# Kernel tuning notes

Measured on AMD Instinct MI355X. Metric: run time of the kernel, lower is better.

## Reference

```python
import jax, jax.numpy as jnp
import numpy as np

N_HEAD = 8
PREFIX_LEN = 77  # hardcoded text prefix length in the 'prefix' model_type branch
MASKED_BIAS = -10000.0


def setup_inputs() -> dict:
    key = jax.random.key(0)
    k1, k2, k3 = jax.random.split(key, 3)
    B, S, D = 8, 1024, 1024
    x = jax.random.normal(k1, (B, S, D), dtype=jnp.float32)
    attention_mask = jnp.zeros((B, 1, 1, S), dtype=jnp.float32)
    W_attn = jax.random.normal(k2, (D, 3 * D), dtype=jnp.float32) * 0.02
    b_attn = jnp.zeros((3 * D,), dtype=jnp.float32)
    W_proj = jax.random.normal(k3, (D, D), dtype=jnp.float32) * 0.02
    b_proj = jnp.zeros((D,), dtype=jnp.float32)
    return {"x": x, "attention_mask": attention_mask, "W_attn": W_attn,
            "b_attn": b_attn, "W_proj": W_proj, "b_proj": b_proj}


def _prefix_mask(S):
    # Rows < 77: attend only to cols < 77 (bidirectional prefix).
    # Rows >= 77: standard causal (cols <= row).
    row = jnp.arange(S)[:, None]
    col = jnp.arange(S)[None, :]
    return jnp.where(row < PREFIX_LEN, col < PREFIX_LEN, col <= row)  # [S, S] bool


def reference(x, attention_mask, W_attn, b_attn, W_proj, b_proj):
    B, S, D = x.shape
    H = N_HEAD
    hd = D // H
    qkv = x @ W_attn + b_attn                         # [B, S, 3D]
    q, k, v = jnp.split(qkv, 3, axis=-1)
    q = q.reshape(B, S, H, hd).transpose(0, 2, 1, 3)  # [B, H, S, hd]
    k = k.reshape(B, S, H, hd).transpose(0, 2, 1, 3)
    v = v.reshape(B, S, H, hd).transpose(0, 2, 1, 3)
    w = jnp.einsum('bhqd,bhkd->bhqk', q, k) / jnp.sqrt(jnp.float32(hd))
    mask = _prefix_mask(S)[None, None]                # [1, 1, S, S]
    w = jnp.where(mask, w, jnp.float32(MASKED_BIAS))
    w = w + attention_mask                            # additive mask [B,1,1,S]
    w = jax.nn.softmax(w, axis=-1)
    # dropout omitted (eval-mode reference)
    a = jnp.einsum('bhqk,bhkd->bhqd', w, v)           # [B, H, S, hd]
    a = a.transpose(0, 2, 1, 3).reshape(B, S, D)      # merge heads
    return a @ W_proj + b_proj
```

## Files before the change

kernel.cpp:

```cpp
#include <hip/hip_runtime.h>
#include <cstdint>
#include <cstddef>

#define B_  8
#define S_  1024
#define D_  1024
#define H_  8
#define HD_ 128
#define N3_ 3072
#define PREFIX 77
#define MASKED_BIAS -10000.0f

typedef __bf16 bf16x8 __attribute__((ext_vector_type(8)));
typedef float  f32x4  __attribute__((ext_vector_type(4)));

__device__ __forceinline__ unsigned short f2bf_rne(float f) {
    unsigned int u = __float_as_uint(f);
    u += 0x7FFFu + ((u >> 16) & 1u);
    return (unsigned short)(u >> 16);
}
__device__ __forceinline__ float bf2f(unsigned short h) {
    return __uint_as_float(((unsigned int)h) << 16);
}

__device__ __forceinline__ void load_lds16(const unsigned short* g, unsigned short* l) {
    __builtin_amdgcn_global_load_lds(
        (const __attribute__((address_space(1))) unsigned int*)g,
        (__attribute__((address_space(3))) unsigned int*)l,
        16, 0, 0);
}

__global__ void prep(const float* __restrict__ x, unsigned short* __restrict__ xb,
                     const float* __restrict__ Wa, unsigned short* __restrict__ wta,
                     const float* __restrict__ Wp, unsigned short* __restrict__ wph) {
    __shared__ float tile[32][33];
    const int bid = (int)blockIdx.x;
    const int tid = threadIdx.x;
    if (bid < 8192) {
        const int i = bid * 256 + tid;
        float4 v = reinterpret_cast<const float4*>(x)[i];
        ushort4 o;
        o.x = f2bf_rne(v.x); o.y = f2bf_rne(v.y); o.z = f2bf_rne(v.z); o.w = f2bf_rne(v.w);
        reinterpret_cast<ushort4*>(xb)[i] = o;
        return;
    }
    const float* in; unsigned short* out; int C, bx, by;
    if (bid < 8192 + 3072) {
        const int lb = bid - 8192;
        in = Wa; out = wta; C = N3_;
        bx = lb % 96; by = lb / 96;
    } else {
        const int lb = bid - 11264;
        in = Wp; out = wph; C = D_;
        bx = lb & 31; by = lb >> 5;
    }
    const int c0 = bx * 32, r0 = by * 32;
    const int tx = tid & 31, ty = tid >> 5;
    #pragma unroll
    for (int i = 0; i < 4; ++i)
        tile[ty + i * 8][tx] = in[(size_t)(r0 + ty + i * 8) * C + c0 + tx];
    __syncthreads();
    #pragma unroll
    for (int i = 0; i < 4; ++i)
        out[(size_t)(c0 + ty + i * 8) * D_ + r0 + tx] = f2bf_rne(tile[tx][ty + i * 8]);
}

__global__ void transpose_v(const unsigned short* __restrict__ v, unsigned short* __restrict__ vt) {
    __shared__ unsigned short tile[32][33];
    const int bh = blockIdx.z;
    const int d0 = blockIdx.x * 32, s0 = blockIdx.y * 32;
    const unsigned short* vi = v + (size_t)bh * S_ * HD_;
    unsigned short* vo = vt + (size_t)bh * S_ * HD_;
    const int tx = threadIdx.x, ty = threadIdx.y;
    #pragma unroll
    for (int i = 0; i < 4; ++i)
        tile[ty + i * 8][tx] = vi[(size_t)(s0 + ty + i * 8) * HD_ + d0 + tx];
    __syncthreads();
    #pragma unroll
    for (int i = 0; i < 4; ++i)
        vo[(size_t)(d0 + ty + i * 8) * S_ + s0 + tx] = tile[tx][ty + i * 8];
}

__global__ __launch_bounds__(256) void gemm_qkv(
    const unsigned short* __restrict__ xb,
    const unsigned short* __restrict__ wt,
    const float* __restrict__ bias,
    unsigned short* __restrict__ qb,
    unsigned short* __restrict__ kb,
    unsigned short* __restrict__ vb) {
    __shared__ unsigned short As[128 * 32];
    __shared__ unsigned short Bs[128 * 32];
    const int tid = threadIdx.x;
    const int bid = (int)blockIdx.x;
    const int xcd = bid & 7, l = bid >> 3;
    const int m0 = (xcd * 8 + (l & 7)) * 128;
    const int n0 = (l >> 3) * 128;
    const int w = tid >> 6, lane = tid & 63;
    const int wm = (w >> 1) * 64, wn = (w & 1) * 64;
    const int l15 = lane & 15, l4 = lane >> 4;
    const int sr = lane >> 2;
    const int sc8 = ((lane & 3) ^ ((lane >> 3) & 3)) * 8;
    const unsigned short* gA0 = xb + (size_t)(m0 + w * 32 + sr) * 1024 + sc8;
    const unsigned short* gA1 = gA0 + 16 * 1024;
    const unsigned short* gB0 = wt + (size_t)(n0 + w * 32 + sr) * 1024 + sc8;
    const unsigned short* gB1 = gB0 + 16 * 1024;
    unsigned short* lA0 = As + w * 1024;
    unsigned short* lA1 = lA0 + 512;
    unsigned short* lB0 = Bs + w * 1024;
    unsigned short* lB1 = lB0 + 512;
    const int ch8 = (l4 ^ ((l15 >> 1) & 3)) * 8;
    f32x4 acc[4][4] = {};
    for (int kt = 0; kt < 32; ++kt) {
        const int k0 = kt * 32;
        __syncthreads();
        load_lds16(gA0 + k0, lA0);
        load_lds16(gA1 + k0, lA1);
        load_lds16(gB0 + k0, lB0);
        load_lds16(gB1 + k0, lB1);
        __syncthreads();
        bf16x8 af[4], bfr[4];
        #pragma unroll
        for (int i = 0; i < 4; ++i) {
            af[i]  = *(const bf16x8*)&As[(wm + i * 16 + l15) * 32 + ch8];
            bfr[i] = *(const bf16x8*)&Bs[(wn + i * 16 + l15) * 32 + ch8];
        }
        #pragma unroll
        for (int mi = 0; mi < 4; ++mi)
            #pragma unroll
            for (int ni = 0; ni < 4; ++ni)
                acc[mi][ni] = __builtin_amdgcn_mfma_f32_16x16x32_bf16(af[mi], bfr[ni], acc[mi][ni], 0, 0, 0);
    }
    #pragma unroll
    for (int mi = 0; mi < 4; ++mi) {
        #pragma unroll
        for (int ni = 0; ni < 4; ++ni) {
            const int col = n0 + wn + ni * 16 + l15;
            const float bv = bias[col];
            const int part = col >> 10;
            const int cidx = col & 1023;
            const int h = cidx >> 7, d = cidx & 127;
            unsigned short* dst = (part == 0) ? qb : ((part == 1) ? kb : vb);
            #pragma unroll
            for (int r = 0; r < 4; ++r) {
                const int row = m0 + wm + mi * 16 + l4 * 4 + r;
                const int b = row >> 10, s = row & 1023;
                dst[((size_t)(b * 8 + h) * 1024 + s) * 128 + d] = f2bf_rne(acc[mi][ni][r] + bv);
            }
        }
    }
}

__global__ __launch_bounds__(256, 2) void attn(
    const unsigned short* __restrict__ qb,
    const unsigned short* __restrict__ kb,
    const unsigned short* __restrict__ vt,
    const float* __restrict__ amask,
    unsigned short* __restrict__ ah,
    unsigned short* __restrict__ al) {
    __shared__ unsigned short Ks[2][64 * 128];
    __shared__ unsigned short Vs[128 * 64];
    __shared__ unsigned short P_lds[4][16 * 72];
    const int tid = threadIdx.x;
    const int w = tid >> 6, lane = tid & 63;
    const int l15 = lane & 15, l4 = lane >> 4;
    const int bidx = (int)blockIdx.x;
    const int qt = 15 - (bidx >> 6);
    const int h = bidx & 7, b = (bidx >> 3) & 7;
    const int bh = b * H_ + h;
    const unsigned short* Q = qb + (size_t)bh * S_ * HD_;
    const unsigned short* Kg = kb + (size_t)bh * S_ * HD_;
    const unsigned short* Vg = vt + (size_t)bh * S_ * HD_;
    unsigned short* pl = P_lds[w];
    const float L2E = 1.44269504088896341f;
    const float SCL = 0.08838834764831845f * L2E;
    const float M2  = 8.0f;

    const int q0 = qt * 64;
    const int q0w = q0 + w * 16;
    bf16x8 qf[4];
    #pragma unroll
    for (int s = 0; s < 4; ++s)
        qf[s] = *(const bf16x8*)(Q + (size_t)(q0w + l15) * 128 + s * 32 + l4 * 8);
    float lsum[4] = {0.f, 0.f, 0.f, 0.f};
    f32x4 o[8] = {};
    const int limit = (q0 + 64 > PREFIX) ? (q0 + 64) : PREFIX;
    const int nkt = (limit + 63) >> 6;

    const int kr = lane >> 4;
    const int kc = lane & 15;
    const int vr = lane >> 3;
    const int vc = lane & 7;

    #pragma unroll
    for (int j = 0; j < 4; ++j) {
        const int rl = w * 16 + j * 4 + kr;
        const int g = kc ^ (j * 4 + kr);
        load_lds16(Kg + (size_t)rl * 128 + g * 8, &Ks[0][(w * 16 + j * 4) * 128]);
    }

    for (int kt = 0; kt < nkt; ++kt) {
        const int kbase = kt * 64;
        const int cur = kt & 1;
        __syncthreads();
        if (kt + 1 < nkt) {
            const int kb2 = (kt + 1) * 64;
            #pragma unroll
            for (int j = 0; j < 4; ++j) {
                const int rl = w * 16 + j * 4 + kr;
                const int g = kc ^ (j * 4 + kr);
                load_lds16(Kg + (size_t)(kb2 + rl) * 128 + g * 8, &Ks[cur ^ 1][(w * 16 + j * 4) * 128]);
            }
        }
        #pragma unroll
        for (int j = 0; j < 4; ++j) {
            const int rv = w * 32 + j * 8 + vr;
            const int g = vc ^ vr;
            load_lds16(Vg + (size_t)rv * 1024 + kbase + g * 8, &Vs[(w * 32 + j * 8) * 64]);
        }
        const bool full = (kbase + 64 <= PREFIX) || (q0w >= PREFIX && kbase + 64 <= q0w);
        #pragma unroll
        for (int t = 0; t < 4; ++t) {
            f32x4 sa = {};
            #pragma unroll
            for (int s = 0; s < 4; ++s) {
                bf16x8 kf = *(const bf16x8*)&Ks[cur][(t * 16 + l15) * 128 + (((s * 4 + l4) ^ l15) * 8)];
                sa = __builtin_amdgcn_mfma_f32_16x16x32_bf16(qf[s], kf, sa, 0, 0, 0);
            }
            const int kcol = kbase + t * 16 + l15;
            const float am = fmaf(amask[b * S_ + kcol], L2E, -M2);
            float p[4];
            if (full) {
                #pragma unroll
                for (int r = 0; r < 4; ++r) p[r] = exp2f(fmaf(sa[r], SCL, am));
            } else {
                #pragma unroll
                for (int r = 0; r < 4; ++r) {
                    const int row = q0w + l4 * 4 + r;
                    const bool keep = (row < PREFIX) ? (kcol < PREFIX) : (kcol <= row);
                    const float e = exp2f(fmaf(sa[r], SCL, am));
                    p[r] = keep ? e : 0.f;
                }
            }
            #pragma unroll
            for (int r = 0; r < 4; ++r) {
                lsum[r] += p[r];
                pl[(l4 * 4 + r) * 72 + t * 16 + l15] = f2bf_rne(p[r]);
            }
        }
        bf16x8 pf0 = *(const bf16x8*)&pl[l15 * 72 + l4 * 8];
        bf16x8 pf1 = *(const bf16x8*)&pl[l15 * 72 + 32 + l4 * 8];
        __syncthreads();
        #pragma unroll
        for (int n = 0; n < 8; ++n) {
            bf16x8 vf = *(const bf16x8*)&Vs[(n * 16 + l15) * 64 + ((l4 ^ (l15 & 7)) * 8)];
            o[n] = __builtin_amdgcn_mfma_f32_16x16x32_bf16(pf0, vf, o[n], 0, 0, 0);
        }
        #pragma unroll
        for (int n = 0; n < 8; ++n) {
            bf16x8 vf = *(const bf16x8*)&Vs[(n * 16 + l15) * 64 + ((((4 + l4) ^ (l15 & 7))) * 8)];
            o[n] = __builtin_amdgcn_mfma_f32_16x16x32_bf16(pf1, vf, o[n], 0, 0, 0);
        }
    }
    float inv_l[4];
    #pragma unroll
    for (int r = 0; r < 4; ++r) {
        float sm = lsum[r];
        sm += __shfl_xor(sm, 1);
        sm += __shfl_xor(sm, 2);
        sm += __shfl_xor(sm, 4);
        sm += __shfl_xor(sm, 8);
        inv_l[r] = 1.0f / sm;
    }
    #pragma unroll
    for (int n = 0; n < 8; ++n) {
        const int d = n * 16 + l15;
        #pragma unroll
        for (int r = 0; r < 4; ++r) {
            const int s = q0w + l4 * 4 + r;
            const float val = o[n][r] * inv_l[r];
            const size_t idx = ((size_t)b * 1024 + s) * 1024 + h * 128 + d;
            unsigned short hv = f2bf_rne(val);
            ah[idx] = hv;
            al[idx] = f2bf_rne(val - bf2f(hv));
        }
    }
}

__global__ __launch_bounds__(256) void gemm_proj(
    const unsigned short* __restrict__ ahp,
    const unsigned short* __restrict__ alp,
    const unsigned short* __restrict__ wh,
    const float* __restrict__ bias,
    float* __restrict__ out) {
    __shared__ unsigned short As[128 * 64];
    __shared__ unsigned short Bs[128 * 64];
    const int tid = threadIdx.x;
    const int bid = (int)blockIdx.x;
    const int xcd = bid & 7, l = bid >> 3;
    const int m0 = (xcd * 8 + (l >> 3)) * 128;
    const int n0 = (l & 7) * 128;
    const int w = tid >> 6, lane = tid & 63;
    const int wm = (w >> 1) * 64, wn = (w & 1) * 64;
    const int l15 = lane & 15, l4 = lane >> 4;
    const int sr = lane >> 3;
    const int sc8 = ((lane & 7) ^ sr) * 8;
    const size_t offA = (size_t)(m0 + w * 32 + sr) * 1024 + sc8;
    const size_t offB = (size_t)(n0 + w * 32 + sr) * 1024 + sc8;
    const unsigned short* gAh = ahp + offA;
    const unsigned short* gAl = alp + offA;
    const unsigned short* gB  = wh + offB;
    unsigned short* lA = As + w * 32 * 64;
    unsigned short* lB = Bs + w * 32 * 64;
    f32x4 acc[4][4] = {};
    for (int kt = 0; kt < 32; ++kt) {
        const int k0 = (kt & 15) * 64;
        const unsigned short* Ap = ((kt & 16) ? gAl : gAh) + k0;
        const unsigned short* Bp = gB + k0;
        __syncthreads();
        #pragma unroll
        for (int j = 0; j < 4; ++j) {
            load_lds16(Ap + j * 8 * 1024, lA + j * 512);
            load_lds16(Bp + j * 8 * 1024, lB + j * 512);
        }
        __syncthreads();
        bf16x8 af[2][4], bfr[2][4];
        #pragma unroll
        for (int kk = 0; kk < 2; ++kk) {
            #pragma unroll
            for (int i = 0; i < 4; ++i) {
                const int cha = ((kk * 4 + l4) ^ (l15 & 7)) * 8;
                af[kk][i]  = *(const bf16x8*)&As[(wm + i * 16 + l15) * 64 + cha];
                bfr[kk][i] = *(const bf16x8*)&Bs[(wn + i * 16 + l15) * 64 + cha];
            }
        }
        #pragma unroll
        for (int kk = 0; kk < 2; ++kk)
            #pragma unroll
            for (int mi = 0; mi < 4; ++mi)
                #pragma unroll
                for (int ni = 0; ni < 4; ++ni)
                    acc[mi][ni] = __builtin_amdgcn_mfma_f32_16x16x32_bf16(af[kk][mi], bfr[kk][ni], acc[mi][ni], 0, 0, 0);
    }
    #pragma unroll
    for (int mi = 0; mi < 4; ++mi) {
        #pragma unroll
        for (int ni = 0; ni < 4; ++ni) {
            const int col = n0 + wn + ni * 16 + l15;
            const float bv = bias[col];
            #pragma unroll
            for (int r = 0; r < 4; ++r) {
                const int row = m0 + wm + mi * 16 + l4 * 4 + r;
                out[(size_t)row * 1024 + col] = acc[mi][ni][r] + bv;
            }
        }
    }
}

extern "C" void kernel_launch(void* const* d_in, const int* in_sizes, int n_in,
                              void* d_out, int out_size, void* d_ws, size_t ws_size,
                              hipStream_t stream) {
    const float* x      = (const float*)d_in[0];
    const float* amask  = (const float*)d_in[1];
    const float* W_attn = (const float*)d_in[2];
    const float* b_attn = (const float*)d_in[3];
    const float* W_proj = (const float*)d_in[4];
    const float* b_proj = (const float*)d_in[5];
    float* out = (float*)d_out;

    char* ws = (char*)d_ws;
    unsigned short* xb  = (unsigned short*)(ws);
    unsigned short* wta = (unsigned short*)(ws + 16777216);
    unsigned short* qb  = (unsigned short*)(ws + 23068672);
    unsigned short* kb2 = (unsigned short*)(ws + 39845888);
    unsigned short* vb  = (unsigned short*)(ws + 56623104);
    unsigned short* vtb = (unsigned short*)(ws + 73400320);
    unsigned short* ahi = (unsigned short*)(ws + 90177536);
    unsigned short* alo = (unsigned short*)(ws + 106954752);
    unsigned short* wph = (unsigned short*)(ws + 123731968);

    prep<<<dim3(12288), 256, 0, stream>>>(x, xb, W_attn, wta, W_proj, wph);
    gemm_qkv<<<dim3(1536), 256, 0, stream>>>(xb, wta, b_attn, qb, kb2, vb);
    transpose_v<<<dim3(HD_ / 32, S_ / 32, B_ * H_), dim3(32, 8), 0, stream>>>(vb, vtb);
    attn<<<dim3(1024), 256, 0, stream>>>(qb, kb2, vtb, amask, ahi, alo);
    gemm_proj<<<dim3(512), 256, 0, stream>>>(ahi, alo, wph, b_proj, out);
}
```

Baseline: 253.0 us.

## Double-buffer QKV GEMM with 256x128 tiles and 8-wave blocks

Restructures the QKV projection GEMM to use 512-thread blocks computing 256x128 output tiles with a K step of 64, split into two 32-wide halves. The LDS is double buffered, so global-to-LDS loads for the next stage are issued while MFMAs run on the current one. Explicit barriers, vmcnt waits and setprio control the schedule. This aims to hide memory latency and raise reuse per block, at the cost of more LDS, fewer blocks and hand-tuned synchronization that is fragile to get right.

```diff
diff --git a/kernel.cpp b/kernel.cpp
--- a/kernel.cpp
+++ b/kernel.cpp
@@ -81,60 +81,84 @@
         vo[(size_t)(d0 + ty + i * 8) * S_ + s0 + tx] = tile[tx][ty + i * 8];
 }
 
-__global__ __launch_bounds__(256) void gemm_qkv(
+__global__ __launch_bounds__(512, 2) void gemm_qkv(
     const unsigned short* __restrict__ xb,
     const unsigned short* __restrict__ wt,
     const float* __restrict__ bias,
     unsigned short* __restrict__ qb,
     unsigned short* __restrict__ kb,
     unsigned short* __restrict__ vb) {
-    __shared__ unsigned short As[128 * 32];
-    __shared__ unsigned short Bs[128 * 32];
+    __shared__ unsigned short As2[2 * 2 * 256 * 32];
+    __shared__ unsigned short Bs2[2 * 2 * 128 * 32];
     const int tid = threadIdx.x;
+    const int w = tid >> 6, lane = tid & 63;
     const int bid = (int)blockIdx.x;
     const int xcd = bid & 7, l = bid >> 3;
-    const int m0 = (xcd * 8 + (l & 7)) * 128;
-    const int n0 = (l >> 3) * 128;
-    const int w = tid >> 6, lane = tid & 63;
-    const int wm = (w >> 1) * 64, wn = (w & 1) * 64;
+    const int m0 = (xcd * 4 + (l & 3)) * 256;
+    const int n0 = (l >> 2) * 128;
+    const int wrow = w >> 1, wcol = w & 1;
     const int l15 = lane & 15, l4 = lane >> 4;
-    const int sr = lane >> 2;
     const int sc8 = ((lane & 3) ^ ((lane >> 3) & 3)) * 8;
-    const unsigned short* gA0 = xb + (size_t)(m0 + w * 32 + sr) * 1024 + sc8;
-    const unsigned short* gA1 = gA0 + 16 * 1024;
-    const unsigned short* gB0 = wt + (size_t)(n0 + w * 32 + sr) * 1024 + sc8;
-    const unsigned short* gB1 = gB0 + 16 * 1024;
-    unsigned short* lA0 = As + w * 1024;
-    unsigned short* lA1 = lA0 + 512;
-    unsigned short* lB0 = Bs + w * 1024;
-    unsigned short* lB1 = lB0 + 512;
+    const size_t gA0 = (size_t)(m0 + w * 16 + (lane >> 2)) * 1024 + sc8;
+    const size_t gA1 = gA0 + (size_t)128 * 1024;
+    const size_t gBo = (size_t)(n0 + w * 16 + (lane >> 2)) * 1024 + sc8;
     const int ch8 = (l4 ^ ((l15 >> 1) & 3)) * 8;
+    int aoff[4], boff[4];
+    #pragma unroll
+    for (int i = 0; i < 4; ++i) {
+        aoff[i] = (wrow * 64 + i * 16 + l15) * 32 + ch8;
+        boff[i] = (wcol * 64 + i * 16 + l15) * 32 + ch8;
+    }
     f32x4 acc[4][4] = {};
-    for (int kt = 0; kt < 32; ++kt) {
-        const int k0 = kt * 32;
-        __syncthreads();
-        load_lds16(gA0 + k0, lA0);
-        load_lds16(gA1 + k0, lA1);
-        load_lds16(gB0 + k0, lB0);
-        load_lds16(gB1 + k0, lB1);
-        __syncthreads();
-        bf16x8 af[4], bfr[4];
-        #pragma unroll
-        for (int i = 0; i < 4; ++i) {
-            af[i]  = *(const bf16x8*)&As[(wm + i * 16 + l15) * 32 + ch8];
-            bfr[i] = *(const bf16x8*)&Bs[(wn + i * 16 + l15) * 32 + ch8];
-        }
-        #pragma unroll
-        for (int mi = 0; mi < 4; ++mi)
-            #pragma unroll
-            for (int ni = 0; ni < 4; ++ni)
-                acc[mi][ni] = __builtin_amdgcn_mfma_f32_16x16x32_bf16(af[mi], bfr[ni], acc[mi][ni], 0, 0, 0);
-    }
+
+#define QSTAGE(DB, KH, KT) do {                                                   \
+    const size_t kc_ = (size_t)((KT) * 64 + (KH) * 32);                           \
+    load_lds16(xb + gA0 + kc_, &As2[((DB) * 2 + (KH)) * 8192 + w * 512]);         \
+    load_lds16(xb + gA1 + kc_, &As2[((DB) * 2 + (KH)) * 8192 + 4096 + w * 512]);  \
+    load_lds16(wt + gBo + kc_, &Bs2[((DB) * 2 + (KH)) * 4096 + w * 512]);         \
+} while (0)
+
+#define QPHASE(DB, KH, STG, WN) do {                                              \
+    bf16x8 af[4], bfr[4];                                                         \
+    _Pragma("unroll") for (int i = 0; i < 4; ++i) {                               \
+        af[i]  = *(const bf16x8*)&As2[((DB) * 2 + (KH)) * 8192 + aoff[i]];        \
+        bfr[i] = *(const bf16x8*)&Bs2[((DB) * 2 + (KH)) * 4096 + boff[i]];        \
+    }                                                                             \
+    STG;                                                                          \
+    asm volatile("s_barrier" ::: "memory");                                       \
+    asm volatile("s_waitcnt lgkmcnt(0)" ::: "memory");                            \
+    __builtin_amdgcn_sched_barrier(0);                                            \
+    __builtin_amdgcn_s_setprio(1);                                                \
+    _Pragma("unroll") for (int mi = 0; mi < 4; ++mi)                              \
+        _Pragma("unroll") for (int ni = 0; ni < 4; ++ni)                          \
+            acc[mi][ni] = __builtin_amdgcn_mfma_f32_16x16x32_bf16(af[mi], bfr[ni], acc[mi][ni], 0, 0, 0); \
+    __builtin_amdgcn_s_setprio(0);                                                \
+    asm volatile("s_waitcnt vmcnt(" WN ")" ::: "memory");                         \
+    asm volatile("s_barrier" ::: "memory");                                       \
+} while (0)
+
+    QSTAGE(0, 0, 0);
+    QSTAGE(0, 1, 0);
+    asm volatile("s_waitcnt vmcnt(3)" ::: "memory");
+    asm volatile("s_barrier" ::: "memory");
+    for (int kt = 0; kt < 14; kt += 2) {
+        QPHASE(0, 0, QSTAGE(1, 0, kt + 1), "3");
+        QPHASE(0, 1, QSTAGE(1, 1, kt + 1), "3");
+        QPHASE(1, 0, QSTAGE(0, 0, kt + 2), "3");
+        QPHASE(1, 1, QSTAGE(0, 1, kt + 2), "3");
+    }
+    QPHASE(0, 0, QSTAGE(1, 0, 15), "3");
+    QPHASE(0, 1, QSTAGE(1, 1, 15), "3");
+    QPHASE(1, 0, (void)0, "0");
+    QPHASE(1, 1, (void)0, "0");
+#undef QSTAGE
+#undef QPHASE
+
     #pragma unroll
     for (int mi = 0; mi < 4; ++mi) {
         #pragma unroll
         for (int ni = 0; ni < 4; ++ni) {
-            const int col = n0 + wn + ni * 16 + l15;
+            const int col = n0 + wcol * 64 + ni * 16 + l15;
             const float bv = bias[col];
             const int part = col >> 10;
             const int cidx = col & 1023;
@@ -142,7 +166,7 @@
             unsigned short* dst = (part == 0) ? qb : ((part == 1) ? kb : vb);
             #pragma unroll
             for (int r = 0; r < 4; ++r) {
-                const int row = m0 + wm + mi * 16 + l4 * 4 + r;
+                const int row = m0 + wrow * 64 + mi * 16 + l4 * 4 + r;
                 const int b = row >> 10, s = row & 1023;
                 dst[((size_t)(b * 8 + h) * 1024 + s) * 128 + d] = f2bf_rne(acc[mi][ni][r] + bv);
             }
@@ -379,7 +403,7 @@
     unsigned short* wph = (unsigned short*)(ws + 123731968);
 
     prep<<<dim3(12288), 256, 0, stream>>>(x, xb, W_attn, wta, W_proj, wph);
-    gemm_qkv<<<dim3(1536), 256, 0, stream>>>(xb, wta, b_attn, qb, kb2, vb);
+    gemm_qkv<<<dim3(768), 512, 0, stream>>>(xb, wta, b_attn, qb, kb2, vb);
     transpose_v<<<dim3(HD_ / 32, S_ / 32, B_ * H_), dim3(32, 8), 0, stream>>>(vb, vtb);
     attn<<<dim3(1024), 256, 0, stream>>>(qb, kb2, vtb, amask, ahi, alo);
     gemm_proj<<<dim3(512), 256, 0, stream>>>(ahi, alo, wph, b_proj, out);
```

Result: slower. 268.5 us (+6.1%).
